# Kernel tuning notes

Hardware: AMD Instinct MI355X
Metric: run time of the kernel (lower is better)

## Reference

```python
import jax, jax.numpy as jnp
import numpy as np

B, N, F, K = 512, 128, 128, 4


def setup_inputs() -> dict:
    key = jax.random.key(0)
    ks = jax.random.split(key, 12)
    # xavier-normal-ish scales
    s_rw = float(np.sqrt(2.0 / (F + F)))
    s_sw = float(np.sqrt(2.0 / (F + F)))
    inp = {
        "H": jax.random.normal(ks[0], (B, N, F), dtype=jnp.float32),
        "E": jax.random.uniform(ks[1], (B, N, N, K), dtype=jnp.float32),
        "RW1": jax.random.normal(ks[2], (F, F, K), dtype=jnp.float32) * s_rw,
        "SW1": jax.random.normal(ks[3], (F, F), dtype=jnp.float32) * s_sw,
        "RW2": jax.random.normal(ks[4], (F, F, K), dtype=jnp.float32) * s_rw,
        "SW2": jax.random.normal(ks[5], (F, F), dtype=jnp.float32) * s_sw,
        "RW3": jax.random.normal(ks[6], (F, F, K), dtype=jnp.float32) * s_rw,
        "SW3": jax.random.normal(ks[7], (F, F), dtype=jnp.float32) * s_sw,
        "W1": jax.random.normal(ks[8], (F, 20), dtype=jnp.float32) * float(np.sqrt(1.0 / F)),
        "b1": jnp.zeros((20,), dtype=jnp.float32),
        "W2": jax.random.normal(ks[9], (20, 1), dtype=jnp.float32) * float(np.sqrt(1.0 / 20)),
        "b2": jnp.zeros((1,), dtype=jnp.float32),
    }
    return inp


def _rgcn_conv(H, E, D, RW, SW):
    # einsum('bi,bijk,bjm,mnk->bin') done in two GEMM-shaped steps
    M = jnp.einsum('bijk,bjm->bimk', E, H)          # [B,N,F,K]
    msg = jnp.einsum('bimk,mnk->bin', M, RW)        # [B,N,F]
    return jax.nn.sigmoid(msg * D[:, :, None] + jnp.einsum('bij,jl->bil', H, SW))


def reference(H, E, RW1, SW1, RW2, SW2, RW3, SW3, W1, b1, W2, b2):
    # degree norm with self-loops: (E + eye)[b,i,:,:].sum() = E.sum((2,3)) + K
    k = jnp.asarray(E.shape[-1], dtype=E.dtype)
    D = 1.0 / (E.sum(axis=(2, 3)) + k)              # [B,N]
    H = _rgcn_conv(H, E, D, RW1, SW1)
    H = _rgcn_conv(H, E, D, RW2, SW2)
    H = _rgcn_conv(H, E, D, RW3, SW3)
    h = jnp.maximum(H @ W1 + b1, 0.1 * (H @ W1 + b1))  # LeakyReLU(0.1)
    score = jnp.mean(jax.nn.sigmoid(h @ W2 + b2))
    return score
```

## Files before the change

kernel.cpp:

```cpp
#include <hip/hip_runtime.h>
#include <math.h>

#define BB 512
#define NN 128
#define FF 128
#define KK 4
#define GS_PITCH 132

typedef __attribute__((ext_vector_type(8))) short bf16x8;
typedef __attribute__((ext_vector_type(4))) float f32x4;

__device__ inline unsigned short f2bf(float x) {
  union { float f; unsigned int u; } v; v.f = x;
  unsigned int r = v.u + 0x7fff + ((v.u >> 16) & 1);
  return (unsigned short)(r >> 16);
}
__device__ inline float bf2f(unsigned short h) {
  union { unsigned int u; float f; } v; v.u = ((unsigned int)h) << 16; return v.f;
}

__device__ inline void g2l16(const unsigned short* gptr, unsigned short* lptr) {
  __builtin_amdgcn_global_load_lds(
      (const __attribute__((address_space(1))) unsigned int*)gptr,
      (__attribute__((address_space(3))) unsigned int*)lptr, 16, 0, 0);
}

__global__ __launch_bounds__(256) void k_prep(
    const float* __restrict__ E, const float* __restrict__ H,
    const float* __restrict__ RW1, const float* __restrict__ SW1,
    const float* __restrict__ RW2, const float* __restrict__ SW2,
    const float* __restrict__ RW3, const float* __restrict__ SW3,
    unsigned short* __restrict__ Eb, unsigned short* __restrict__ Ha,
    unsigned short* __restrict__ W2L, float* __restrict__ Dv,
    float* __restrict__ Sum, int* __restrict__ Cnt)
{
  const int bid = blockIdx.x;
  if (bid < 16384) {
    int wave = threadIdx.x >> 6;
    int lane = threadIdx.x & 63;
    int row  = bid * 4 + wave;
    const float* p = E + (size_t)row * 512 + lane * 8;
    f32x4 a = *(const f32x4*)p;
    f32x4 b = *(const f32x4*)(p + 4);
    float s = a[0] + a[1] + a[2] + a[3] + b[0] + b[1] + b[2] + b[3];
    #pragma unroll
    for (int off = 32; off > 0; off >>= 1) s += __shfl_down(s, off, 64);
    if (lane == 0) Dv[row] = 1.0f / (s + 4.0f);
    union { unsigned short h[8]; f32x4 v; } u;
    u.h[0] = f2bf(a[0]); u.h[1] = f2bf(a[1]); u.h[2] = f2bf(a[2]); u.h[3] = f2bf(a[3]);
    u.h[4] = f2bf(b[0]); u.h[5] = f2bf(b[1]); u.h[6] = f2bf(b[2]); u.h[7] = f2bf(b[3]);
    *(f32x4*)(Eb + (size_t)row * 512 + lane * 8) = u.v;
  } else if (bid < 20480) {
    size_t i = ((size_t)(bid - 16384) * 256 + threadIdx.x) * 8;
    f32x4 a = *(const f32x4*)(H + i);
    f32x4 b = *(const f32x4*)(H + i + 4);
    union { unsigned short h[8]; f32x4 v; } u;
    u.h[0] = f2bf(a[0]); u.h[1] = f2bf(a[1]); u.h[2] = f2bf(a[2]); u.h[3] = f2bf(a[3]);
    u.h[4] = f2bf(b[0]); u.h[5] = f2bf(b[1]); u.h[6] = f2bf(b[2]); u.h[7] = f2bf(b[3]);
    *(f32x4*)(Ha + i) = u.v;
  } else {
    int t2  = bid - 20480;
    int tab = t2 / 320;
    int idx = (t2 - tab * 320) * 256 + threadIdx.x;
    int m = idx & 127;
    int c = idx >> 7;
    const float* RW = (tab == 0) ? RW1 : (tab == 1) ? RW2 : RW3;
    const float* SW = (tab == 0) ? SW1 : (tab == 1) ? SW2 : SW3;
    float v = (c < 512) ? RW[m * 512 + c] : SW[m * 128 + (c - 512)];
    W2L[(size_t)tab * 81920 + idx] = f2bf(v);
    if (t2 == 0 && threadIdx.x == 0) { *Sum = 0.0f; *Cnt = 0; }
  }
}

__device__ __forceinline__ void layer_body(
    const unsigned short* __restrict__ E_b,
    const unsigned short* __restrict__ H_b,
    const unsigned short* __restrict__ W2c,
    const float* __restrict__ dvb,
    unsigned short* __restrict__ O_b,
    unsigned short* Gs, unsigned short* Es, const int tid)
{
  const int w = tid >> 6, l = tid & 63;
  const int wr = w >> 1, wc = w & 1;
  const int lq = l >> 4, lm = l & 15;

  f32x4 macc[2][4] = {};

  for (int s = 0; s < 4; ++s) {
    if (s) __syncthreads();

    bf16x8 fa0[4], fb0[2];
    #pragma unroll
    for (int f = 0; f < 4; ++f)
      fa0[f] = *(const bf16x8*)(W2c + (w * 64 + f * 16 + lm) * 128 + lq * 8);
    #pragma unroll
    for (int g = 0; g < 2; ++g)
      fb0[g] = *(const bf16x8*)(H_b + (s * 32 + g * 16 + lm) * 128 + lq * 8);

    #pragma unroll
    for (int r = 0; r < 4; ++r) {
      int R   = r * 32 + w * 4 + (l >> 4);
      int cbg = (l & 15) ^ (R & 15);
      g2l16(E_b + R * 512 + s * 128 + cbg * 8,
            Es + (r * 32 + w * 4) * 128);
    }

    f32x4 gacc[4][2] = {};
    #pragma unroll
    for (int f = 0; f < 4; ++f)
      #pragma unroll
      for (int g = 0; g < 2; ++g)
        gacc[f][g] = __builtin_amdgcn_mfma_f32_16x16x32_bf16(fa0[f], fb0[g], gacc[f][g], 0, 0, 0);
    #pragma unroll
    for (int k0 = 32; k0 < 128; k0 += 32) {
      bf16x8 fa[4], fb[2];
      #pragma unroll
      for (int f = 0; f < 4; ++f)
        fa[f] = *(const bf16x8*)(W2c + (w * 64 + f * 16 + lm) * 128 + k0 + lq * 8);
      #pragma unroll
      for (int g = 0; g < 2; ++g)
        fb[g] = *(const bf16x8*)(H_b + (s * 32 + g * 16 + lm) * 128 + k0 + lq * 8);
      #pragma unroll
      for (int f = 0; f < 4; ++f)
        #pragma unroll
        for (int g = 0; g < 2; ++g)
          gacc[f][g] = __builtin_amdgcn_mfma_f32_16x16x32_bf16(fa[f], fb[g], gacc[f][g], 0, 0, 0);
    }
    #pragma unroll
    for (int f = 0; f < 4; ++f) {
      int n = w * 16 + f * 4 + lq;
      #pragma unroll
      for (int g = 0; g < 2; ++g) {
        int jl = g * 16 + lm;
        union { unsigned short h4[4]; uint2 v; } u;
        u.h4[0] = f2bf(gacc[f][g][0]); u.h4[1] = f2bf(gacc[f][g][1]);
        u.h4[2] = f2bf(gacc[f][g][2]); u.h4[3] = f2bf(gacc[f][g][3]);
        *(uint2*)(&Gs[n * GS_PITCH + jl * 4]) = u.v;
      }
    }
    __syncthreads();

    #pragma unroll
    for (int kt = 0; kt < 4; ++kt) {
      bf16x8 ea[2], fb[4];
      #pragma unroll
      for (int f = 0; f < 2; ++f) {
        int i  = wr * 32 + f * 16 + lm;
        int cb = (kt * 4 + lq) ^ lm;
        ea[f] = *(const bf16x8*)(Es + i * 128 + cb * 8);
      }
      #pragma unroll
      for (int g = 0; g < 4; ++g)
        fb[g] = *(const bf16x8*)(&Gs[(wc * 64 + g * 16 + lm) * GS_PITCH + kt * 32 + lq * 8]);
      #pragma unroll
      for (int f = 0; f < 2; ++f)
        #pragma unroll
        for (int g = 0; g < 4; ++g)
          macc[f][g] = __builtin_amdgcn_mfma_f32_16x16x32_bf16(ea[f], fb[g], macc[f][g], 0, 0, 0);
    }
  }

  f32x4 sacc[2][4] = {};
  #pragma unroll
  for (int k0 = 0; k0 < 128; k0 += 32) {
    bf16x8 fa[2], fb[4];
    #pragma unroll
    for (int f = 0; f < 2; ++f)
      fa[f] = *(const bf16x8*)(H_b + (wr * 32 + f * 16 + lm) * 128 + k0 + lq * 8);
    #pragma unroll
    for (int g = 0; g < 4; ++g)
      fb[g] = *(const bf16x8*)(W2c + (512 + wc * 64 + g * 16 + lm) * 128 + k0 + lq * 8);
    #pragma unroll
    for (int f = 0; f < 2; ++f)
      #pragma unroll
      for (int g = 0; g < 4; ++g)
        sacc[f][g] = __builtin_amdgcn_mfma_f32_16x16x32_bf16(fa[f], fb[g], sacc[f][g], 0, 0, 0);
  }

  __syncthreads();
  #pragma unroll
  for (int f = 0; f < 2; ++f) {
    int i0 = wr * 32 + f * 16 + lq * 4;
    f32x4 d = *(const f32x4*)(dvb + i0);
    #pragma unroll
    for (int g = 0; g < 4; ++g) {
      int n = wc * 64 + g * 16 + lm;
      #pragma unroll
      for (int r = 0; r < 4; ++r) {
        float v = fmaf(macc[f][g][r], d[r], sacc[f][g][r]);
        Es[(i0 + r) * 128 + n] = f2bf(1.0f / (1.0f + __expf(-v)));
      }
    }
  }
  __syncthreads();
  {
    int off = tid * 32;
    f32x4 v0 = *(const f32x4*)(Es + off);
    f32x4 v1 = *(const f32x4*)(Es + off + 8);
    f32x4 v2 = *(const f32x4*)(Es + off + 16);
    f32x4 v3 = *(const f32x4*)(Es + off + 24);
    *(f32x4*)(O_b + off)      = v0;
    *(f32x4*)(O_b + off + 8)  = v1;
    *(f32x4*)(O_b + off + 16) = v2;
    *(f32x4*)(O_b + off + 24) = v3;
  }
  __syncthreads();
}

__global__ __launch_bounds__(512, 2) void k_mega(
    const unsigned short* __restrict__ Eb,
    const unsigned short* __restrict__ Ha,
    unsigned short* __restrict__ Hb,
    unsigned short* __restrict__ Hc,
    unsigned short* __restrict__ Hd,
    const unsigned short* __restrict__ W2L,
    const float* __restrict__ Dv,
    const float* __restrict__ W1, const float* __restrict__ b1,
    const float* __restrict__ W2w, const float* __restrict__ b2,
    float* __restrict__ Sum, int* __restrict__ Cnt,
    float* __restrict__ out)
{
  __shared__ unsigned short Gs[128 * GS_PITCH];
  __shared__ unsigned short Es[128 * 128];

  const int b = blockIdx.x;
  const int tid = threadIdx.x;
  const unsigned short* E_b = Eb + (size_t)b * 65536;
  const float* dvb = Dv + b * 128;

  layer_body(E_b, Ha + (size_t)b * 16384, W2L,          dvb, Hb + (size_t)b * 16384, Gs, Es, tid);
  layer_body(E_b, Hb + (size_t)b * 16384, W2L + 81920,  dvb, Hc + (size_t)b * 16384, Gs, Es, tid);
  layer_body(E_b, Hc + (size_t)b * 16384, W2L + 163840, dvb, Hd + (size_t)b * 16384, Gs, Es, tid);

  float* W1s = (float*)Gs;
  float* b1s = W1s + 2560;
  float* W2s = b1s + 32;
  float* red = W2s + 32;
  for (int i = tid; i < 2560; i += 512) W1s[i] = W1[i];
  if (tid < 20) { b1s[tid] = b1[tid]; W2s[tid] = W2w[tid]; }
  __syncthreads();

  float s = 0.0f;
  if (tid < 128) {
    const unsigned short* hr = Hd + (size_t)(b * 128 + tid) * 128;
    float h[20];
    #pragma unroll
    for (int j = 0; j < 20; ++j) h[j] = b1s[j];
    for (int m8 = 0; m8 < 128; m8 += 8) {
      f32x4 pk = *(const f32x4*)(hr + m8);
      const unsigned short* us = (const unsigned short*)&pk;
      #pragma unroll
      for (int e = 0; e < 8; ++e) {
        float x = bf2f(us[e]);
        #pragma unroll
        for (int j = 0; j < 20; ++j) h[j] = fmaf(x, W1s[(m8 + e) * 20 + j], h[j]);
      }
    }
    float v = b2[0];
    #pragma unroll
    for (int j = 0; j < 20; ++j) {
      float t = h[j];
      t = fmaxf(t, 0.1f * t);
      v = fmaf(t, W2s[j], v);
    }
    s = 1.0f / (1.0f + __expf(-v));
  }

  red[tid] = s;
  __syncthreads();
  #pragma unroll
  for (int off = 256; off > 0; off >>= 1) {
    if (tid < off) red[tid] += red[tid + off];
    __syncthreads();
  }
  if (tid == 0) {
    atomicAdd(Sum, red[0]);
    __threadfence();
    int v = atomicAdd(Cnt, 1);
    if (v == BB - 1) {
      float tot = atomicAdd(Sum, 0.0f);
      out[0] = tot * (1.0f / 65536.0f);
    }
  }
}

extern "C" void kernel_launch(void* const* d_in, const int* in_sizes, int n_in,
                              void* d_out, int out_size, void* d_ws, size_t ws_size,
                              hipStream_t stream) {
  (void)in_sizes; (void)n_in; (void)out_size; (void)ws_size;
  const float* H   = (const float*)d_in[0];
  const float* E   = (const float*)d_in[1];
  const float* RW1 = (const float*)d_in[2];
  const float* SW1 = (const float*)d_in[3];
  const float* RW2 = (const float*)d_in[4];
  const float* SW2 = (const float*)d_in[5];
  const float* RW3 = (const float*)d_in[6];
  const float* SW3 = (const float*)d_in[7];
  const float* W1  = (const float*)d_in[8];
  const float* b1  = (const float*)d_in[9];
  const float* W2  = (const float*)d_in[10];
  const float* b2  = (const float*)d_in[11];
  float* out = (float*)d_out;

  char* w = (char*)d_ws;
  float*          wsD   = (float*)w;           w += (size_t)65536 * 4;
  unsigned short* wsEb  = (unsigned short*)w;  w += (size_t)33554432 * 2;
  unsigned short* wsHa  = (unsigned short*)w;  w += (size_t)8388608 * 2;
  unsigned short* wsHb  = (unsigned short*)w;  w += (size_t)8388608 * 2;
  unsigned short* wsHc  = (unsigned short*)w;  w += (size_t)8388608 * 2;
  unsigned short* wsHd  = (unsigned short*)w;  w += (size_t)8388608 * 2;
  unsigned short* wsW2  = (unsigned short*)w;  w += (size_t)3 * 81920 * 2;
  float*          wsSum = (float*)w;           w += 64;
  int*            wsCnt = (int*)w;             w += 64;

  k_prep<<<21440, 256, 0, stream>>>(E, H, RW1, SW1, RW2, SW2, RW3, SW3,
                                    wsEb, wsHa, wsW2, wsD, wsSum, wsCnt);
  k_mega<<<BB, 512, 0, stream>>>(wsEb, wsHa, wsHb, wsHc, wsHd, wsW2, wsD,
                                 W1, b1, W2, b2, wsSum, wsCnt, out);
}
```

Baseline: 503.1 us.

## Split mega-kernel into per-layer kernels with global G intermediate and direct-from-global MFMA operands

After: 545.2 us. +8.4%, slower.

```diff
diff --git a/kernel.cpp b/kernel.cpp
--- a/kernel.cpp
+++ b/kernel.cpp
@@ -5,7 +5,6 @@
 #define NN 128
 #define FF 128
 #define KK 4
-#define GS_PITCH 132
 
 typedef __attribute__((ext_vector_type(8))) short bf16x8;
 typedef __attribute__((ext_vector_type(4))) float f32x4;
@@ -17,12 +16,6 @@
 }
 __device__ inline float bf2f(unsigned short h) {
   union { unsigned int u; float f; } v; v.u = ((unsigned int)h) << 16; return v.f;
-}
-
-__device__ inline void g2l16(const unsigned short* gptr, unsigned short* lptr) {
-  __builtin_amdgcn_global_load_lds(
-      (const __attribute__((address_space(1))) unsigned int*)gptr,
-      (__attribute__((address_space(3))) unsigned int*)lptr, 16, 0, 0);
 }
 
 __global__ __launch_bounds__(256) void k_prep(
@@ -72,92 +65,95 @@
   }
 }
 
-__device__ __forceinline__ void layer_body(
-    const unsigned short* __restrict__ E_b,
+__device__ __forceinline__ void gA_body(
     const unsigned short* __restrict__ H_b,
-    const unsigned short* __restrict__ W2c,
-    const float* __restrict__ dvb,
-    unsigned short* __restrict__ O_b,
-    unsigned short* Gs, unsigned short* Es, const int tid)
+    const unsigned short* __restrict__ W2,
+    unsigned short* __restrict__ G_b,
+    int tid)
 {
+  const int w = tid >> 6, l = tid & 63;
+  const int lq = l >> 4, lm = l & 15;
+
+  bf16x8 fa[4][4];
+  #pragma unroll
+  for (int f = 0; f < 4; ++f)
+    #pragma unroll
+    for (int k0 = 0; k0 < 4; ++k0)
+      fa[f][k0] = *(const bf16x8*)(W2 + (w * 64 + f * 16 + lm) * 128 + k0 * 32 + lq * 8);
+
+  #pragma unroll 2
+  for (int g = 0; g < 8; ++g) {
+    bf16x8 fbk[4];
+    #pragma unroll
+    for (int k0 = 0; k0 < 4; ++k0)
+      fbk[k0] = *(const bf16x8*)(H_b + (g * 16 + lm) * 128 + k0 * 32 + lq * 8);
+    f32x4 gacc[4] = {};
+    #pragma unroll
+    for (int k0 = 0; k0 < 4; ++k0)
+      #pragma unroll
+      for (int f = 0; f < 4; ++f)
+        gacc[f] = __builtin_amdgcn_mfma_f32_16x16x32_bf16(fa[f][k0], fbk[k0], gacc[f], 0, 0, 0);
+    #pragma unroll
+    for (int f = 0; f < 4; ++f) {
+      int n = w * 16 + f * 4 + lq;
+      union { unsigned short h4[4]; uint2 v; } u;
+      u.h4[0] = f2bf(gacc[f][0]); u.h4[1] = f2bf(gacc[f][1]);
+      u.h4[2] = f2bf(gacc[f][2]); u.h4[3] = f2bf(gacc[f][3]);
+      *(uint2*)(G_b + (size_t)n * 512 + (g * 16 + lm) * 4) = u.v;
+    }
+  }
+}
+
+__global__ __launch_bounds__(512, 2) void k_gA(
+    const unsigned short* __restrict__ Hin,
+    const unsigned short* __restrict__ W2,
+    unsigned short* __restrict__ Gt)
+{
+  const int b = blockIdx.x;
+  gA_body(Hin + (size_t)b * 16384, W2, Gt + (size_t)b * 65536, threadIdx.x);
+}
+
+template<int FUSEA, int DOMLP>
+__global__ __launch_bounds__(512, 2) void k_gB(
+    const unsigned short* __restrict__ Eb,
+    const unsigned short* __restrict__ Gin,
+    const unsigned short* __restrict__ Hin,
+    const unsigned short* __restrict__ W2cur,
+    const unsigned short* __restrict__ W2nxt,
+    const float* __restrict__ Dv,
+    unsigned short* __restrict__ Hout,
+    unsigned short* __restrict__ Gout,
+    const float* __restrict__ W1, const float* __restrict__ b1,
+    const float* __restrict__ W2w, const float* __restrict__ b2,
+    float* __restrict__ Sum, int* __restrict__ Cnt, float* __restrict__ out)
+{
+  __shared__ unsigned short Os[128 * 128];
+
+  const int b = blockIdx.x, tid = threadIdx.x;
   const int w = tid >> 6, l = tid & 63;
   const int wr = w >> 1, wc = w & 1;
   const int lq = l >> 4, lm = l & 15;
 
+  const unsigned short* E_b = Eb  + (size_t)b * 65536;
+  const unsigned short* G_b = Gin + (size_t)b * 65536;
+  const unsigned short* H_b = Hin + (size_t)b * 16384;
+  unsigned short*       O_b = Hout + (size_t)b * 16384;
+
   f32x4 macc[2][4] = {};
-
-  for (int s = 0; s < 4; ++s) {
-    if (s) __syncthreads();
-
-    bf16x8 fa0[4], fb0[2];
-    #pragma unroll
-    for (int f = 0; f < 4; ++f)
-      fa0[f] = *(const bf16x8*)(W2c + (w * 64 + f * 16 + lm) * 128 + lq * 8);
-    #pragma unroll
-    for (int g = 0; g < 2; ++g)
-      fb0[g] = *(const bf16x8*)(H_b + (s * 32 + g * 16 + lm) * 128 + lq * 8);
-
-    #pragma unroll
-    for (int r = 0; r < 4; ++r) {
-      int R   = r * 32 + w * 4 + (l >> 4);
-      int cbg = (l & 15) ^ (R & 15);
-      g2l16(E_b + R * 512 + s * 128 + cbg * 8,
-            Es + (r * 32 + w * 4) * 128);
-    }
-
-    f32x4 gacc[4][2] = {};
-    #pragma unroll
-    for (int f = 0; f < 4; ++f)
-      #pragma unroll
-      for (int g = 0; g < 2; ++g)
-        gacc[f][g] = __builtin_amdgcn_mfma_f32_16x16x32_bf16(fa0[f], fb0[g], gacc[f][g], 0, 0, 0);
-    #pragma unroll
-    for (int k0 = 32; k0 < 128; k0 += 32) {
-      bf16x8 fa[4], fb[2];
-      #pragma unroll
-      for (int f = 0; f < 4; ++f)
-        fa[f] = *(const bf16x8*)(W2c + (w * 64 + f * 16 + lm) * 128 + k0 + lq * 8);
-      #pragma unroll
-      for (int g = 0; g < 2; ++g)
-        fb[g] = *(const bf16x8*)(H_b + (s * 32 + g * 16 + lm) * 128 + k0 + lq * 8);
-      #pragma unroll
-      for (int f = 0; f < 4; ++f)
-        #pragma unroll
-        for (int g = 0; g < 2; ++g)
-          gacc[f][g] = __builtin_amdgcn_mfma_f32_16x16x32_bf16(fa[f], fb[g], gacc[f][g], 0, 0, 0);
-    }
-    #pragma unroll
-    for (int f = 0; f < 4; ++f) {
-      int n = w * 16 + f * 4 + lq;
-      #pragma unroll
-      for (int g = 0; g < 2; ++g) {
-        int jl = g * 16 + lm;
-        union { unsigned short h4[4]; uint2 v; } u;
-        u.h4[0] = f2bf(gacc[f][g][0]); u.h4[1] = f2bf(gacc[f][g][1]);
-        u.h4[2] = f2bf(gacc[f][g][2]); u.h4[3] = f2bf(gacc[f][g][3]);
-        *(uint2*)(&Gs[n * GS_PITCH + jl * 4]) = u.v;
-      }
-    }
-    __syncthreads();
-
-    #pragma unroll
-    for (int kt = 0; kt < 4; ++kt) {
-      bf16x8 ea[2], fb[4];
-      #pragma unroll
-      for (int f = 0; f < 2; ++f) {
-        int i  = wr * 32 + f * 16 + lm;
-        int cb = (kt * 4 + lq) ^ lm;
-        ea[f] = *(const bf16x8*)(Es + i * 128 + cb * 8);
-      }
+  #pragma unroll 4
+  for (int kt = 0; kt < 16; ++kt) {
+    bf16x8 ea[2], fb[4];
+    #pragma unroll
+    for (int f = 0; f < 2; ++f)
+      ea[f] = *(const bf16x8*)(E_b + (size_t)(wr * 32 + f * 16 + lm) * 512 + kt * 32 + lq * 8);
+    #pragma unroll
+    for (int g = 0; g < 4; ++g)
+      fb[g] = *(const bf16x8*)(G_b + (size_t)(wc * 64 + g * 16 + lm) * 512 + kt * 32 + lq * 8);
+    #pragma unroll
+    for (int f = 0; f < 2; ++f)
       #pragma unroll
       for (int g = 0; g < 4; ++g)
-        fb[g] = *(const bf16x8*)(&Gs[(wc * 64 + g * 16 + lm) * GS_PITCH + kt * 32 + lq * 8]);
-      #pragma unroll
-      for (int f = 0; f < 2; ++f)
-        #pragma unroll
-        for (int g = 0; g < 4; ++g)
-          macc[f][g] = __builtin_amdgcn_mfma_f32_16x16x32_bf16(ea[f], fb[g], macc[f][g], 0, 0, 0);
-    }
+        macc[f][g] = __builtin_amdgcn_mfma_f32_16x16x32_bf16(ea[f], fb[g], macc[f][g], 0, 0, 0);
   }
 
   f32x4 sacc[2][4] = {};
@@ -169,7 +165,7 @@
       fa[f] = *(const bf16x8*)(H_b + (wr * 32 + f * 16 + lm) * 128 + k0 + lq * 8);
     #pragma unroll
     for (int g = 0; g < 4; ++g)
-      fb[g] = *(const bf16x8*)(W2c + (512 + wc * 64 + g * 16 + lm) * 128 + k0 + lq * 8);
+      fb[g] = *(const bf16x8*)(W2cur + (512 + wc * 64 + g * 16 + lm) * 128 + k0 + lq * 8);
     #pragma unroll
     for (int f = 0; f < 2; ++f)
       #pragma unroll
@@ -177,7 +173,7 @@
         sacc[f][g] = __builtin_amdgcn_mfma_f32_16x16x32_bf16(fa[f], fb[g], sacc[f][g], 0, 0, 0);
   }
 
-  __syncthreads();
+  const float* dvb = Dv + b * 128;
   #pragma unroll
   for (int f = 0; f < 2; ++f) {
     int i0 = wr * 32 + f * 16 + lq * 4;
@@ -188,98 +184,79 @@
       #pragma unroll
       for (int r = 0; r < 4; ++r) {
         float v = fmaf(macc[f][g][r], d[r], sacc[f][g][r]);
-        Es[(i0 + r) * 128 + n] = f2bf(1.0f / (1.0f + __expf(-v)));
+        Os[(i0 + r) * 128 + n] = f2bf(1.0f / (1.0f + __expf(-v)));
       }
     }
   }
   __syncthreads();
   {
     int off = tid * 32;
-    f32x4 v0 = *(const f32x4*)(Es + off);
-    f32x4 v1 = *(const f32x4*)(Es + off + 8);
-    f32x4 v2 = *(const f32x4*)(Es + off + 16);
-    f32x4 v3 = *(const f32x4*)(Es + off + 24);
+    f32x4 v0 = *(const f32x4*)(Os + off);
+    f32x4 v1 = *(const f32x4*)(Os + off + 8);
+    f32x4 v2 = *(const f32x4*)(Os + off + 16);
+    f32x4 v3 = *(const f32x4*)(Os + off + 24);
     *(f32x4*)(O_b + off)      = v0;
     *(f32x4*)(O_b + off + 8)  = v1;
     *(f32x4*)(O_b + off + 16) = v2;
     *(f32x4*)(O_b + off + 24) = v3;
   }
-  __syncthreads();
-}
-
-__global__ __launch_bounds__(512, 2) void k_mega(
-    const unsigned short* __restrict__ Eb,
-    const unsigned short* __restrict__ Ha,
-    unsigned short* __restrict__ Hb,
-    unsigned short* __restrict__ Hc,
-    unsigned short* __restrict__ Hd,
-    const unsigned short* __restrict__ W2L,
-    const float* __restrict__ Dv,
-    const float* __restrict__ W1, const float* __restrict__ b1,
-    const float* __restrict__ W2w, const float* __restrict__ b2,
-    float* __restrict__ Sum, int* __restrict__ Cnt,
-    float* __restrict__ out)
-{
-  __shared__ unsigned short Gs[128 * GS_PITCH];
-  __shared__ unsigned short Es[128 * 128];
-
-  const int b = blockIdx.x;
-  const int tid = threadIdx.x;
-  const unsigned short* E_b = Eb + (size_t)b * 65536;
-  const float* dvb = Dv + b * 128;
-
-  layer_body(E_b, Ha + (size_t)b * 16384, W2L,          dvb, Hb + (size_t)b * 16384, Gs, Es, tid);
-  layer_body(E_b, Hb + (size_t)b * 16384, W2L + 81920,  dvb, Hc + (size_t)b * 16384, Gs, Es, tid);
-  layer_body(E_b, Hc + (size_t)b * 16384, W2L + 163840, dvb, Hd + (size_t)b * 16384, Gs, Es, tid);
-
-  float* W1s = (float*)Gs;
-  float* b1s = W1s + 2560;
-  float* W2s = b1s + 32;
-  float* red = W2s + 32;
-  for (int i = tid; i < 2560; i += 512) W1s[i] = W1[i];
-  if (tid < 20) { b1s[tid] = b1[tid]; W2s[tid] = W2w[tid]; }
-  __syncthreads();
-
-  float s = 0.0f;
-  if (tid < 128) {
-    const unsigned short* hr = Hd + (size_t)(b * 128 + tid) * 128;
-    float h[20];
-    #pragma unroll
-    for (int j = 0; j < 20; ++j) h[j] = b1s[j];
-    for (int m8 = 0; m8 < 128; m8 += 8) {
-      f32x4 pk = *(const f32x4*)(hr + m8);
-      const unsigned short* us = (const unsigned short*)&pk;
-      #pragma unroll
-      for (int e = 0; e < 8; ++e) {
-        float x = bf2f(us[e]);
+
+  if (FUSEA) {
+    __syncthreads();
+    gA_body(O_b, W2nxt, Gout + (size_t)b * 65536, tid);
+  }
+
+  if (DOMLP) {
+    __syncthreads();
+    float* W1s = (float*)Os;
+    float* b1s = W1s + 2560;
+    float* W2s = b1s + 32;
+    float* red = W2s + 32;
+    for (int i = tid; i < 2560; i += 512) W1s[i] = W1[i];
+    if (tid < 20) { b1s[tid] = b1[tid]; W2s[tid] = W2w[tid]; }
+    __syncthreads();
+
+    float s = 0.0f;
+    if (tid < 128) {
+      const unsigned short* hr = O_b + (size_t)tid * 128;
+      float h[20];
+      #pragma unroll
+      for (int j = 0; j < 20; ++j) h[j] = b1s[j];
+      for (int m8 = 0; m8 < 128; m8 += 8) {
+        f32x4 pk = *(const f32x4*)(hr + m8);
+        const unsigned short* us = (const unsigned short*)&pk;
         #pragma unroll
-        for (int j = 0; j < 20; ++j) h[j] = fmaf(x, W1s[(m8 + e) * 20 + j], h[j]);
+        for (int e = 0; e < 8; ++e) {
+          float x = bf2f(us[e]);
+          #pragma unroll
+          for (int j = 0; j < 20; ++j) h[j] = fmaf(x, W1s[(m8 + e) * 20 + j], h[j]);
+        }
       }
-    }
-    float v = b2[0];
-    #pragma unroll
-    for (int j = 0; j < 20; ++j) {
-      float t = h[j];
-      t = fmaxf(t, 0.1f * t);
-      v = fmaf(t, W2s[j], v);
-    }
-    s = 1.0f / (1.0f + __expf(-v));
-  }
-
-  red[tid] = s;
-  __syncthreads();
-  #pragma unroll
-  for (int off = 256; off > 0; off >>= 1) {
-    if (tid < off) red[tid] += red[tid + off];
+      float v = b2[0];
+      #pragma unroll
+      for (int j = 0; j < 20; ++j) {
+        float t = h[j];
+        t = fmaxf(t, 0.1f * t);
+        v = fmaf(t, W2s[j], v);
+      }
+      s = 1.0f / (1.0f + __expf(-v));
+    }
+
+    red[tid] = s;
     __syncthreads();
-  }
-  if (tid == 0) {
-    atomicAdd(Sum, red[0]);
-    __threadfence();
-    int v = atomicAdd(Cnt, 1);
-    if (v == BB - 1) {
-      float tot = atomicAdd(Sum, 0.0f);
-      out[0] = tot * (1.0f / 65536.0f);
+    #pragma unroll
+    for (int off = 256; off > 0; off >>= 1) {
+      if (tid < off) red[tid] += red[tid + off];
+      __syncthreads();
+    }
+    if (tid == 0) {
+      atomicAdd(Sum, red[0]);
+      __threadfence();
+      int v = atomicAdd(Cnt, 1);
+      if (v == BB - 1) {
+        float tot = atomicAdd(Sum, 0.0f);
+        out[0] = tot * (1.0f / 65536.0f);
+      }
     }
   }
 }
@@ -305,6 +282,8 @@
   char* w = (char*)d_ws;
   float*          wsD   = (float*)w;           w += (size_t)65536 * 4;
   unsigned short* wsEb  = (unsigned short*)w;  w += (size_t)33554432 * 2;
+  unsigned short* wsG1  = (unsigned short*)w;  w += (size_t)33554432 * 2;
+  unsigned short* wsG2  = (unsigned short*)w;  w += (size_t)33554432 * 2;
   unsigned short* wsHa  = (unsigned short*)w;  w += (size_t)8388608 * 2;
   unsigned short* wsHb  = (unsigned short*)w;  w += (size_t)8388608 * 2;
   unsigned short* wsHc  = (unsigned short*)w;  w += (size_t)8388608 * 2;
@@ -315,6 +294,16 @@
 
   k_prep<<<21440, 256, 0, stream>>>(E, H, RW1, SW1, RW2, SW2, RW3, SW3,
                                     wsEb, wsHa, wsW2, wsD, wsSum, wsCnt);
-  k_mega<<<BB, 512, 0, stream>>>(wsEb, wsHa, wsHb, wsHc, wsHd, wsW2, wsD,
-                                 W1, b1, W2, b2, wsSum, wsCnt, out);
-}
+
+  k_gA<<<BB, 512, 0, stream>>>(wsHa, wsW2, wsG1);
+
+  k_gB<1, 0><<<BB, 512, 0, stream>>>(wsEb, wsG1, wsHa, wsW2, wsW2 + 81920,
+                                     wsD, wsHb, wsG2,
+                                     W1, b1, W2, b2, wsSum, wsCnt, out);
+  k_gB<1, 0><<<BB, 512, 0, stream>>>(wsEb, wsG2, wsHb, wsW2 + 81920, wsW2 + 163840,
+                                     wsD, wsHc, wsG1,
+                                     W1, b1, W2, b2, wsSum, wsCnt, out);
+  k_gB<0, 1><<<BB, 512, 0, stream>>>(wsEb, wsG1, wsHc, wsW2 + 163840, wsW2,
+                                     wsD, wsHd, wsG2,
+                                     W1, b1, W2, b2, wsSum, wsCnt, out);
+}
```

## Split fused three-layer mega kernel into per-layer kernel launches

Applied to the files above, without the earlier changes.

Result: faster. 428.0 us (-14.9%).

```diff
diff --git a/kernel.cpp b/kernel.cpp
--- a/kernel.cpp
+++ b/kernel.cpp
@@ -72,14 +72,25 @@
   }
 }
 
-__device__ __forceinline__ void layer_body(
-    const unsigned short* __restrict__ E_b,
-    const unsigned short* __restrict__ H_b,
-    const unsigned short* __restrict__ W2c,
-    const float* __restrict__ dvb,
-    unsigned short* __restrict__ O_b,
-    unsigned short* Gs, unsigned short* Es, const int tid)
+template<int DOMLP>
+__global__ __launch_bounds__(512, 2) void k_layer(
+    const unsigned short* __restrict__ Eb,
+    const unsigned short* __restrict__ Hin,
+    const unsigned short* __restrict__ W2L,
+    const float* __restrict__ Dv,
+    unsigned short* __restrict__ Hout,
+    const float* __restrict__ W1, const float* __restrict__ b1,
+    const float* __restrict__ W2w, const float* __restrict__ b2,
+    float* __restrict__ Sum, int* __restrict__ Cnt, float* __restrict__ out)
 {
+  __shared__ unsigned short Gs[128 * GS_PITCH];
+  __shared__ unsigned short Es[128 * 128];
+
+  const int b = blockIdx.x;
+  const unsigned short* E_b = Eb  + (size_t)b * 65536;
+  const unsigned short* H_b = Hin + (size_t)b * 16384;
+
+  const int tid = threadIdx.x;
   const int w = tid >> 6, l = tid & 63;
   const int wr = w >> 1, wc = w & 1;
   const int lq = l >> 4, lm = l & 15;
@@ -92,7 +103,7 @@
     bf16x8 fa0[4], fb0[2];
     #pragma unroll
     for (int f = 0; f < 4; ++f)
-      fa0[f] = *(const bf16x8*)(W2c + (w * 64 + f * 16 + lm) * 128 + lq * 8);
+      fa0[f] = *(const bf16x8*)(W2L + (w * 64 + f * 16 + lm) * 128 + lq * 8);
     #pragma unroll
     for (int g = 0; g < 2; ++g)
       fb0[g] = *(const bf16x8*)(H_b + (s * 32 + g * 16 + lm) * 128 + lq * 8);
@@ -116,7 +127,7 @@
       bf16x8 fa[4], fb[2];
       #pragma unroll
       for (int f = 0; f < 4; ++f)
-        fa[f] = *(const bf16x8*)(W2c + (w * 64 + f * 16 + lm) * 128 + k0 + lq * 8);
+        fa[f] = *(const bf16x8*)(W2L + (w * 64 + f * 16 + lm) * 128 + k0 + lq * 8);
       #pragma unroll
       for (int g = 0; g < 2; ++g)
         fb[g] = *(const bf16x8*)(H_b + (s * 32 + g * 16 + lm) * 128 + k0 + lq * 8);
@@ -169,7 +180,7 @@
       fa[f] = *(const bf16x8*)(H_b + (wr * 32 + f * 16 + lm) * 128 + k0 + lq * 8);
     #pragma unroll
     for (int g = 0; g < 4; ++g)
-      fb[g] = *(const bf16x8*)(W2c + (512 + wc * 64 + g * 16 + lm) * 128 + k0 + lq * 8);
+      fb[g] = *(const bf16x8*)(W2L + (512 + wc * 64 + g * 16 + lm) * 128 + k0 + lq * 8);
     #pragma unroll
     for (int f = 0; f < 2; ++f)
       #pragma unroll
@@ -177,6 +188,7 @@
         sacc[f][g] = __builtin_amdgcn_mfma_f32_16x16x32_bf16(fa[f], fb[g], sacc[f][g], 0, 0, 0);
   }
 
+  const float* dvb = Dv + b * 128;
   __syncthreads();
   #pragma unroll
   for (int f = 0; f < 2; ++f) {
@@ -193,6 +205,7 @@
     }
   }
   __syncthreads();
+  unsigned short* O_b = Hout + (size_t)b * 16384;
   {
     int off = tid * 32;
     f32x4 v0 = *(const f32x4*)(Es + off);
@@ -204,82 +217,58 @@
     *(f32x4*)(O_b + off + 16) = v2;
     *(f32x4*)(O_b + off + 24) = v3;
   }
-  __syncthreads();
-}
-
-__global__ __launch_bounds__(512, 2) void k_mega(
-    const unsigned short* __restrict__ Eb,
-    const unsigned short* __restrict__ Ha,
-    unsigned short* __restrict__ Hb,
-    unsigned short* __restrict__ Hc,
-    unsigned short* __restrict__ Hd,
-    const unsigned short* __restrict__ W2L,
-    const float* __restrict__ Dv,
-    const float* __restrict__ W1, const float* __restrict__ b1,
-    const float* __restrict__ W2w, const float* __restrict__ b2,
-    float* __restrict__ Sum, int* __restrict__ Cnt,
-    float* __restrict__ out)
-{
-  __shared__ unsigned short Gs[128 * GS_PITCH];
-  __shared__ unsigned short Es[128 * 128];
-
-  const int b = blockIdx.x;
-  const int tid = threadIdx.x;
-  const unsigned short* E_b = Eb + (size_t)b * 65536;
-  const float* dvb = Dv + b * 128;
-
-  layer_body(E_b, Ha + (size_t)b * 16384, W2L,          dvb, Hb + (size_t)b * 16384, Gs, Es, tid);
-  layer_body(E_b, Hb + (size_t)b * 16384, W2L + 81920,  dvb, Hc + (size_t)b * 16384, Gs, Es, tid);
-  layer_body(E_b, Hc + (size_t)b * 16384, W2L + 163840, dvb, Hd + (size_t)b * 16384, Gs, Es, tid);
-
-  float* W1s = (float*)Gs;
-  float* b1s = W1s + 2560;
-  float* W2s = b1s + 32;
-  float* red = W2s + 32;
-  for (int i = tid; i < 2560; i += 512) W1s[i] = W1[i];
-  if (tid < 20) { b1s[tid] = b1[tid]; W2s[tid] = W2w[tid]; }
-  __syncthreads();
-
-  float s = 0.0f;
-  if (tid < 128) {
-    const unsigned short* hr = Hd + (size_t)(b * 128 + tid) * 128;
-    float h[20];
-    #pragma unroll
-    for (int j = 0; j < 20; ++j) h[j] = b1s[j];
-    for (int m8 = 0; m8 < 128; m8 += 8) {
-      f32x4 pk = *(const f32x4*)(hr + m8);
-      const unsigned short* us = (const unsigned short*)&pk;
-      #pragma unroll
-      for (int e = 0; e < 8; ++e) {
-        float x = bf2f(us[e]);
+
+  if (DOMLP) {
+    __syncthreads();
+    float* W1s = (float*)Gs;
+    float* b1s = W1s + 2560;
+    float* W2s = b1s + 32;
+    float* red = W2s + 32;
+    for (int i = tid; i < 2560; i += 512) W1s[i] = W1[i];
+    if (tid < 20) { b1s[tid] = b1[tid]; W2s[tid] = W2w[tid]; }
+    __syncthreads();
+
+    float sv = 0.0f;
+    if (tid < 128) {
+      const unsigned short* hr = O_b + (size_t)tid * 128;
+      float h[20];
+      #pragma unroll
+      for (int j = 0; j < 20; ++j) h[j] = b1s[j];
+      for (int m8 = 0; m8 < 128; m8 += 8) {
+        f32x4 pk = *(const f32x4*)(hr + m8);
+        const unsigned short* us = (const unsigned short*)&pk;
         #pragma unroll
-        for (int j = 0; j < 20; ++j) h[j] = fmaf(x, W1s[(m8 + e) * 20 + j], h[j]);
-      }
-    }
-    float v = b2[0];
-    #pragma unroll
-    for (int j = 0; j < 20; ++j) {
-      float t = h[j];
-      t = fmaxf(t, 0.1f * t);
-      v = fmaf(t, W2s[j], v);
-    }
-    s = 1.0f / (1.0f + __expf(-v));
-  }
-
-  red[tid] = s;
-  __syncthreads();
-  #pragma unroll
-  for (int off = 256; off > 0; off >>= 1) {
-    if (tid < off) red[tid] += red[tid + off];
+        for (int e = 0; e < 8; ++e) {
+          float x = bf2f(us[e]);
+          #pragma unroll
+          for (int j = 0; j < 20; ++j) h[j] = fmaf(x, W1s[(m8 + e) * 20 + j], h[j]);
+        }
+      }
+      float v = b2[0];
+      #pragma unroll
+      for (int j = 0; j < 20; ++j) {
+        float t = h[j];
+        t = fmaxf(t, 0.1f * t);
+        v = fmaf(t, W2s[j], v);
+      }
+      sv = 1.0f / (1.0f + __expf(-v));
+    }
+
+    red[tid] = sv;
     __syncthreads();
-  }
-  if (tid == 0) {
-    atomicAdd(Sum, red[0]);
-    __threadfence();
-    int v = atomicAdd(Cnt, 1);
-    if (v == BB - 1) {
-      float tot = atomicAdd(Sum, 0.0f);
-      out[0] = tot * (1.0f / 65536.0f);
+    #pragma unroll
+    for (int off = 256; off > 0; off >>= 1) {
+      if (tid < off) red[tid] += red[tid + off];
+      __syncthreads();
+    }
+    if (tid == 0) {
+      atomicAdd(Sum, red[0]);
+      __threadfence();
+      int c = atomicAdd(Cnt, 1);
+      if (c == BB - 1) {
+        float tot = atomicAdd(Sum, 0.0f);
+        out[0] = tot * (1.0f / 65536.0f);
+      }
     }
   }
 }
@@ -315,6 +304,11 @@
 
   k_prep<<<21440, 256, 0, stream>>>(E, H, RW1, SW1, RW2, SW2, RW3, SW3,
                                     wsEb, wsHa, wsW2, wsD, wsSum, wsCnt);
-  k_mega<<<BB, 512, 0, stream>>>(wsEb, wsHa, wsHb, wsHc, wsHd, wsW2, wsD,
-                                 W1, b1, W2, b2, wsSum, wsCnt, out);
-}
+
+  k_layer<0><<<BB, 512, 0, stream>>>(wsEb, wsHa, wsW2,          wsD, wsHb,
+                                     W1, b1, W2, b2, wsSum, wsCnt, out);
+  k_layer<0><<<BB, 512, 0, stream>>>(wsEb, wsHb, wsW2 + 81920,  wsD, wsHc,
+                                     W1, b1, W2, b2, wsSum, wsCnt, out);
+  k_layer<1><<<BB, 512, 0, stream>>>(wsEb, wsHc, wsW2 + 163840, wsD, wsHd,
+                                     W1, b1, W2, b2, wsSum, wsCnt, out);
+}
```
